# Performance work log

Measured on AMD Instinct MI355X. Metric: run time of the kernel, lower is better.

Reference implementation:

```python
import jax, jax.numpy as jnp
import numpy as np

N = 65536   # number of GP locations
M = 64      # max ancestor set size (contiguous window A(i) = {i-M+1..i})
B = 16384   # minibatch size


def setup_inputs() -> dict:
    rng = np.random.default_rng(0)
    i = np.arange(N)
    # CSR row lengths: U (lower-tri) row i has cols {max(0,i-M+1)..i}; V (upper-tri) row j has cols {j..min(j+M-1,N-1)}
    row_len_u = np.minimum(i + 1, M)
    row_len_v = np.minimum(M, N - i)
    crow_u = np.concatenate([[0], np.cumsum(row_len_u)]).astype(np.int32)
    crow_v = np.concatenate([[0], np.cumsum(row_len_v)]).astype(np.int32)
    nnz = int(crow_u[-1])  # 4192288, same for both matrices
    # off-diagonals small, diagonals near 1 (kept positive for logDet and solve stability)
    U_values = (rng.standard_normal(nnz) * 0.1).astype(np.float32)
    U_values[crow_u[1:] - 1] = rng.uniform(0.8, 1.2, N).astype(np.float32)  # last entry of row i = (i,i)
    V_values = (rng.standard_normal(nnz) * 0.1).astype(np.float32)
    V_values[crow_v[:-1]] = rng.uniform(0.8, 1.2, N).astype(np.float32)    # first entry of row i = (i,i)
    mean = (rng.standard_normal(N) * 0.5).astype(np.float32)
    mean_post = (rng.standard_normal(N) * 0.5).astype(np.float32)
    y = rng.standard_normal(N).astype(np.float32)
    mini_indices = rng.integers(0, N, B).astype(np.int32)
    return {
        'U_values': jnp.asarray(U_values),
        'V_values': jnp.asarray(V_values),
        'mean': jnp.asarray(mean),
        'mean_post': jnp.asarray(mean_post),
        'y': jnp.asarray(y),
        'noise': jnp.float32(0.1),
        'mini_indices': jnp.asarray(mini_indices),
        'crow_u': jnp.asarray(crow_u),
        'crow_v': jnp.asarray(crow_v),
    }


def reference(U_values, V_values, mean, mean_post, y, noise, mini_indices, crow_u, crow_v):
    nnz = U_values.shape[0]
    g = mini_indices                       # [B] selected rows
    L = jnp.minimum(g + 1, M)              # n_anc per selected row
    p = jnp.arange(M)
    valid = p[None, :] >= (M - L)[:, None]                 # [B,M] right-aligned validity mask
    anc = g[:, None] - (M - 1 - p)[None, :]                # global ancestor index at padded slot p
    anc_c = jnp.clip(anc, 0, N - 1)

    # get_sub_rows(UTrans): row g entries at A(g), right-aligned into [B,M]
    u_idx = crow_u[g][:, None] + (p[None, :] - (M - L)[:, None])
    U_sub = jnp.where(valid, U_values[jnp.clip(u_idx, 0, nnz - 1)], 0.0)

    # ragged mean difference gather (masked scatter in the original)
    md = jnp.where(valid, (mean - mean_post)[anc_c], 0.0)  # [B,M]

    # get_sub_mat(V, unit_diag=True): V[A(g),A(g)] bottom-right aligned, identity padding
    jrow = anc_c[:, :, None]                               # global row index of block row r
    icol = anc_c[:, None, :]                               # global col index of block col c
    vidx = crow_v[jrow] + (icol - jrow)                    # CSR value index of V[jrow, icol]
    blk_mask = (valid[:, :, None] & valid[:, None, :]
                & (p[None, :, None] <= p[None, None, :]))  # upper-tri of active block
    eye = jnp.eye(M, dtype=U_values.dtype)
    V_sub = jnp.where(blk_mask, V_values[jnp.clip(vidx, 0, nnz - 1)], eye[None, :, :])  # [B,M,M]

    # batched triangular solves
    ej = jnp.zeros((B, M), U_values.dtype).at[:, -1].set(1.0)
    sol_e = jax.scipy.linalg.solve_triangular(V_sub, ej[:, :, None], lower=False)
    marginalVarPost = jnp.sum(sol_e * sol_e, axis=(1, 2))  # [B]
    sol_u = jax.scipy.linalg.solve_triangular(V_sub, U_sub[:, :, None], lower=False)
    innerCov = -0.5 * jnp.sum(sol_u * sol_u)

    innerMean = -0.5 * jnp.sum(jnp.sum(U_sub * md, axis=1) ** 2)

    # log-determinant terms from diagonal gathers
    logDet = (jnp.sum(jnp.log(U_values[crow_u[g + 1] - 1]))
              - jnp.sum(jnp.log(V_values[crow_v[g]])))

    # Gaussian expected likelihood (noise is not None branch)
    resid = y[g] - mean_post[g]
    ell = (-0.5 * B * jnp.log(2.0 * jnp.pi * noise)
           - (jnp.sum(resid * resid) + jnp.sum(marginalVarPost)) / (2.0 * noise))

    return logDet + innerMean + innerCov + ell
```

## Files before the change

### kernel.cpp

```cpp
#include <hip/hip_runtime.h>
#include <math.h>

constexpr int kN = 65536;
constexpr int kB = 16384;
constexpr int kTileW = 2560;

static __device__ __forceinline__ float bcastf(float v, int lane) {
    union { float f; int i; } u;
    u.f = v;
    u.i = __builtin_amdgcn_readlane(u.i, lane);
    return u.f;
}

static __device__ __forceinline__ void gload_lds16(const float* g, float* l) {
    __builtin_amdgcn_global_load_lds(
        (const __attribute__((address_space(1))) void*)g,
        (__attribute__((address_space(3))) void*)l, 16, 0, 0);
}
static __device__ __forceinline__ void gload_lds4(const float* g, float* l) {
    __builtin_amdgcn_global_load_lds(
        (const __attribute__((address_space(1))) void*)g,
        (__attribute__((address_space(3))) void*)l, 4, 0, 0);
}

static __device__ __forceinline__ int row_start(int j) {
    const int t = j >> 4;
    return 1024 * t - 128 * t * (t - 1) + (64 - 16 * t) * (j - 16 * t);
}

static __device__ __forceinline__ bool is_hot(int g) {
    return (g >= 63) && (g <= kN - 63);
}

__global__ __launch_bounds__(64) void gp_solve_kernel(
    const float* __restrict__ Uv,
    const float* __restrict__ Vv,
    const float* __restrict__ mean,
    const float* __restrict__ mean_post,
    const float* __restrict__ y,
    const int*   __restrict__ gidx,
    const int*   __restrict__ crow_u,
    const int*   __restrict__ crow_v,
    const float* __restrict__ noise,
    float*       __restrict__ partial)
{
    __shared__ __align__(16) float myl[kTileW];

    const int lane = (int)threadIdx.x;
    const int b    = (int)blockIdx.x;
    const int g    = gidx[b];

    const int  anc = g - 63 + lane;
    const bool vl  = (anc >= 0);

    const int L  = (g + 1 < 64) ? (g + 1) : 64;
    const int ub = (g >= 63) ? (2016 + 64 * (g - 63)) : crow_u[g];

    float uval = 0.0f, md = 0.0f;
    if (vl) {
        uval = Uv[ub + lane - (64 - L)];
        md   = mean[anc] - mean_post[anc];
    }
    const float yg  = y[g];
    const float mpg = mean_post[g];

    if (is_hot(g)) {
        const float* base = Vv + 64 * (g - 63);
        {
            const float* src = base + 4 * lane;
            #pragma unroll
            for (int k = 0; k < 4; ++k)
                gload_lds16(src + 256 * k, myl + 256 * k);
        }
        #pragma unroll
        for (int k = 0; k < 3; ++k) {
            const int w   = 256 * k + 4 * lane;
            const int jj  = ((w >> 4) * 171) >> 9;
            const int col = w - 48 * jj;
            gload_lds16(base + 64 * (16 + jj) + col, myl + 1024 + 256 * k);
        }
        #pragma unroll
        for (int k = 0; k < 2; ++k) {
            const int w = 256 * k + 4 * lane;
            gload_lds16(base + 64 * (32 + (w >> 5)) + (w & 31), myl + 1792 + 256 * k);
        }
        {
            const int w = 4 * lane;
            gload_lds16(base + 64 * (48 + (w >> 4)) + (w & 15), myl + 2304);
        }
    } else {
        int rowbase = 0;
        if (vl) rowbase = crow_v[anc];
        for (int j = 0; j < 64; ++j) {
            const int rbj = __builtin_amdgcn_readlane(rowbase, j);
            const int dst = row_start(j);
            if (lane < 64 - j) {
                if (g - 63 + j >= 0)
                    gload_lds4(Vv + rbj + lane, myl + dst);
                else
                    myl[dst + lane] = 0.0f;
            }
        }
    }
    asm volatile("s_waitcnt vmcnt(0) lgkmcnt(0)" ::: "memory");

    const int rs = row_start(lane);
    const float d0   = myl[rs];
    const float diag = vl ? d0 : 1.0f;
    const float invd = 1.0f / diag;

    const float* vrow = myl + (rs - lane);
    float v[64];
    #pragma unroll
    for (int i = 0; i < 64; i += 2) {
        const float a0 = vrow[i];
        const float a1 = vrow[i + 1];
        v[i]     = a0 * invd;
        v[i + 1] = a1 * invd;
    }

    float r_e = (lane == 63) ? invd : 0.0f;
    float r_u = uval * invd;
    float acc_e = 0.0f, acc_u = 0.0f;

    #pragma unroll
    for (int i = 63; i >= 0; --i) {
        const float s_e = bcastf(r_e, i);
        const float s_u = bcastf(r_u, i);
        r_e = fmaf(-v[i], s_e, r_e);
        r_u = fmaf(-v[i], s_u, r_u);
        acc_e = fmaf(s_e, s_e, acc_e);
        acc_u = fmaf(s_u, s_u, acc_u);
    }

    float dot = uval * md;
    #pragma unroll
    for (int m = 1; m < 64; m <<= 1)
        dot += __shfl_xor(dot, m, 64);

    const float ulast  = bcastf(uval, 63);
    const float vfirst = bcastf(diag, 63);

    if (lane == 0) {
        const float resid = yg - mpg;
        const float inv2n = 0.5f / noise[0];
        partial[b] = __logf(ulast) - __logf(vfirst)
                   - 0.5f * dot * dot
                   - 0.5f * acc_u
                   - (resid * resid + acc_e) * inv2n;
    }
}

__global__ __launch_bounds__(1024) void gp_reduce_kernel(
    const float* __restrict__ partial,
    const float* __restrict__ noise,
    float*       __restrict__ out)
{
    __shared__ float ws[16];
    const int t = (int)threadIdx.x;
    float a = 0.0f;
    #pragma unroll
    for (int k = 0; k < 4; ++k) {
        const float4 p = reinterpret_cast<const float4*>(partial)[t + 1024 * k];
        a += (p.x + p.y) + (p.z + p.w);
    }
    #pragma unroll
    for (int m = 1; m < 64; m <<= 1)
        a += __shfl_xor(a, m, 64);
    if ((t & 63) == 0) ws[t >> 6] = a;
    __syncthreads();
    if (t == 0) {
        float tot = 0.0f;
        #pragma unroll
        for (int k = 0; k < 16; ++k) tot += ws[k];
        tot += -0.5f * (float)kB * logf(2.0f * 3.14159265358979323846f * noise[0]);
        out[0] = tot;
    }
}

extern "C" void kernel_launch(void* const* d_in, const int* in_sizes, int n_in,
                              void* d_out, int out_size, void* d_ws, size_t ws_size,
                              hipStream_t stream)
{
    const float* Uv        = (const float*)d_in[0];
    const float* Vv        = (const float*)d_in[1];
    const float* mean      = (const float*)d_in[2];
    const float* mean_post = (const float*)d_in[3];
    const float* y         = (const float*)d_in[4];
    const float* noise     = (const float*)d_in[5];
    const int*   gidx      = (const int*)d_in[6];
    const int*   crow_u    = (const int*)d_in[7];
    const int*   crow_v    = (const int*)d_in[8];
    float* partial = (float*)d_ws;

    gp_solve_kernel<<<dim3(kB), dim3(64), 0, stream>>>(
        Uv, Vv, mean, mean_post, y, gidx, crow_u, crow_v, noise, partial);
    gp_reduce_kernel<<<dim3(1), dim3(1024), 0, stream>>>(
        partial, noise, (float*)d_out);
}
```

Baseline: 36.94 us.

## Bucket minibatch rows by index range to share V tiles across solves

Adds a single-block counting sort that groups minibatch indices into 1024 buckets of 64 rows. Each bucket block loads one contiguous 8192-float V slab into LDS and runs all of its rows' triangular solves from that slab, instead of every row fetching its own 64x64 window. Tail-bucket rows go to a separate per-row cold kernel capped at 512 entries, and the final reduce is shrunk. This removes redundant global traffic for overlapping windows, at the cost of two extra launches, a serial sort block, and load imbalance across buckets. If more than 512 indices land in the last bucket, the overflow is silently dropped.

New measurement: 53.06 us. 1.44x slower.

```diff
diff --git a/kernel.cpp b/kernel.cpp
--- a/kernel.cpp
+++ b/kernel.cpp
@@ -3,6 +3,9 @@
 
 constexpr int kN = 65536;
 constexpr int kB = 16384;
+constexpr int kNB = 1024;
+constexpr int kBufW = 8192;
+constexpr int kColdCap = 512;
 constexpr int kTileW = 2560;
 
 static __device__ __forceinline__ float bcastf(float v, int lane) {
@@ -27,34 +30,198 @@
     const int t = j >> 4;
     return 1024 * t - 128 * t * (t - 1) + (64 - 16 * t) * (j - 16 * t);
 }
-
 static __device__ __forceinline__ bool is_hot(int g) {
     return (g >= 63) && (g <= kN - 63);
 }
 
-__global__ __launch_bounds__(64) void gp_solve_kernel(
+__global__ __launch_bounds__(1024) void gp_sort_kernel(
+    const int* __restrict__ gidx,
+    int* __restrict__ sortedg, int* __restrict__ start,
+    int* __restrict__ coldg, int* __restrict__ coldcnt)
+{
+    __shared__ int hist[kNB];
+    __shared__ int wsum[16];
+    __shared__ int coldc;
+    const int t = (int)threadIdx.x, lane = t & 63, w = t >> 6;
+    hist[t] = 0;
+    if (t == 0) coldc = 0;
+    __syncthreads();
+    int gs[16];
+    #pragma unroll
+    for (int k = 0; k < 16; ++k) {
+        gs[k] = gidx[t + 1024 * k];
+        const int bkt = gs[k] >> 6;
+        if (bkt < kNB - 1) atomicAdd(&hist[bkt], 1);
+    }
+    __syncthreads();
+    const int v = hist[t];
+    int x = v;
+    #pragma unroll
+    for (int d = 1; d < 64; d <<= 1) {
+        const int nn = __shfl_up(x, d, 64);
+        if (lane >= d) x += nn;
+    }
+    if (lane == 63) wsum[w] = x;
+    __syncthreads();
+    if (t == 0) {
+        int acc = 0;
+        #pragma unroll
+        for (int k = 0; k < 16; ++k) { const int sv = wsum[k]; wsum[k] = acc; acc += sv; }
+    }
+    __syncthreads();
+    const int excl = x - v + wsum[w];
+    start[t] = excl;
+    if (t == kNB - 1) start[kNB] = excl + v;
+    __syncthreads();
+    hist[t] = excl;
+    __syncthreads();
+    #pragma unroll
+    for (int k = 0; k < 16; ++k) {
+        const int g = gs[k], bkt = g >> 6;
+        if (bkt < kNB - 1) {
+            const int p = atomicAdd(&hist[bkt], 1);
+            sortedg[p] = g;
+        } else {
+            const int p = atomicAdd(&coldc, 1);
+            if (p < kColdCap) coldg[p] = g;
+        }
+    }
+    __syncthreads();
+    if (t == 0) coldcnt[0] = (coldc < kColdCap) ? coldc : kColdCap;
+}
+
+__global__ __launch_bounds__(256) void gp_bucket_kernel(
     const float* __restrict__ Uv,
     const float* __restrict__ Vv,
     const float* __restrict__ mean,
     const float* __restrict__ mean_post,
     const float* __restrict__ y,
-    const int*   __restrict__ gidx,
+    const int*   __restrict__ crow_u,
+    const float* __restrict__ noise,
+    const int*   __restrict__ sortedg,
+    const int*   __restrict__ start,
+    float*       __restrict__ partial)
+{
+    __shared__ __align__(16) float buf[kBufW];
+    __shared__ float cred[4];
+
+    const int tid  = (int)threadIdx.x, lane = tid & 63, wid = tid >> 6;
+    const int bid  = (int)blockIdx.x;
+    const int b    = ((bid & 7) << 7) | (bid >> 3);
+    const int s    = start[b];
+    const int n    = start[b + 1] - s;
+    if (n == 0) { if (tid == 0) partial[b] = 0.0f; return; }
+
+    const float inv2n = 0.5f / noise[0];
+
+    if (b > 0) {
+        const float* src = Vv + 64 * (64 * b - 63);
+        #pragma unroll
+        for (int k = 0; k < 8; ++k) {
+            const int ow = 1024 * k + 256 * wid;
+            gload_lds16(src + ow + 4 * lane, buf + ow);
+        }
+    } else {
+        #pragma unroll
+        for (int k = 0; k < 8; ++k) {
+            const int wd = 1024 * k + 4 * tid;
+            float4 val = make_float4(0.0f, 0.0f, 0.0f, 0.0f);
+            if (wd >= 4032)
+                val = *reinterpret_cast<const float4*>(Vv + (wd - 4032));
+            *reinterpret_cast<float4*>(buf + wd) = val;
+        }
+    }
+    asm volatile("s_waitcnt vmcnt(0) lgkmcnt(0)" ::: "memory");
+    __syncthreads();
+
+    float accum = 0.0f;
+    for (int e = wid; e < n; e += 4) {
+        const int g   = sortedg[s + e];
+        const int off = g - 64 * b;
+        const int anc = g - 63 + lane;
+        const bool vl = (anc >= 0);
+        const int  L  = (g + 1 < 64) ? (g + 1) : 64;
+        const int  ub = (g >= 63) ? (2016 + 64 * (g - 63)) : crow_u[g];
+
+        float uval = 0.0f, md = 0.0f;
+        if (vl) {
+            uval = Uv[ub + lane - (64 - L)];
+            md   = mean[anc] - mean_post[anc];
+        }
+        const float yv  = y[g];
+        const float mpv = mean_post[g];
+
+        const int l = off + lane;
+        const float d0 = buf[64 * l];
+        const float invd = vl ? (1.0f / d0) : 0.0f;
+
+        const float* vrow = buf + (64 * l - lane);
+        float v[64];
+        #pragma unroll
+        for (int i = 0; i < 64; i += 2) {
+            const float a0 = vrow[i];
+            const float a1 = vrow[i + 1];
+            v[i]     = a0 * invd;
+            v[i + 1] = a1 * invd;
+        }
+
+        float r_e = (lane == 63) ? invd : 0.0f;
+        float r_u = uval * invd;
+        float acc_e = 0.0f, acc_u = 0.0f;
+        #pragma unroll
+        for (int i = 63; i >= 0; --i) {
+            const float s_e = bcastf(r_e, i);
+            const float s_u = bcastf(r_u, i);
+            r_e = fmaf(-v[i], s_e, r_e);
+            r_u = fmaf(-v[i], s_u, r_u);
+            acc_e = fmaf(s_e, s_e, acc_e);
+            acc_u = fmaf(s_u, s_u, acc_u);
+        }
+
+        float dot = uval * md;
+        #pragma unroll
+        for (int m = 1; m < 64; m <<= 1)
+            dot += __shfl_xor(dot, m, 64);
+
+        const float ulast  = bcastf(uval, 63);
+        const float vfirst = bcastf(d0, 63);
+        const float resid  = yv - mpv;
+        accum += __logf(ulast) - __logf(vfirst)
+               - 0.5f * dot * dot
+               - 0.5f * acc_u
+               - (resid * resid + acc_e) * inv2n;
+    }
+
+    if (lane == 0) cred[wid] = accum;
+    __syncthreads();
+    if (tid == 0)
+        partial[b] = (cred[0] + cred[1]) + (cred[2] + cred[3]);
+}
+
+__global__ __launch_bounds__(64) void gp_cold_kernel(
+    const float* __restrict__ Uv,
+    const float* __restrict__ Vv,
+    const float* __restrict__ mean,
+    const float* __restrict__ mean_post,
+    const float* __restrict__ y,
     const int*   __restrict__ crow_u,
     const int*   __restrict__ crow_v,
     const float* __restrict__ noise,
-    float*       __restrict__ partial)
+    const int*   __restrict__ coldg,
+    const int*   __restrict__ coldcnt,
+    float*       __restrict__ partialC)
 {
     __shared__ __align__(16) float myl[kTileW];
-
     const int lane = (int)threadIdx.x;
-    const int b    = (int)blockIdx.x;
-    const int g    = gidx[b];
+    const int i    = (int)blockIdx.x;
+    const int cnt  = coldcnt[0];
+    if (i >= cnt) { if (lane == 0) partialC[i] = 0.0f; return; }
+    const int g = coldg[i];
 
     const int  anc = g - 63 + lane;
     const bool vl  = (anc >= 0);
-
-    const int L  = (g + 1 < 64) ? (g + 1) : 64;
-    const int ub = (g >= 63) ? (2016 + 64 * (g - 63)) : crow_u[g];
+    const int  L   = (g + 1 < 64) ? (g + 1) : 64;
+    const int  ub  = (g >= 63) ? (2016 + 64 * (g - 63)) : crow_u[g];
 
     float uval = 0.0f, md = 0.0f;
     if (vl) {
@@ -66,12 +233,9 @@
 
     if (is_hot(g)) {
         const float* base = Vv + 64 * (g - 63);
-        {
-            const float* src = base + 4 * lane;
-            #pragma unroll
-            for (int k = 0; k < 4; ++k)
-                gload_lds16(src + 256 * k, myl + 256 * k);
-        }
+        { const float* src = base + 4 * lane;
+          #pragma unroll
+          for (int k = 0; k < 4; ++k) gload_lds16(src + 256 * k, myl + 256 * k); }
         #pragma unroll
         for (int k = 0; k < 3; ++k) {
             const int w   = 256 * k + 4 * lane;
@@ -84,10 +248,8 @@
             const int w = 256 * k + 4 * lane;
             gload_lds16(base + 64 * (32 + (w >> 5)) + (w & 31), myl + 1792 + 256 * k);
         }
-        {
-            const int w = 4 * lane;
-            gload_lds16(base + 64 * (48 + (w >> 4)) + (w & 15), myl + 2304);
-        }
+        { const int w = 4 * lane;
+          gload_lds16(base + 64 * (48 + (w >> 4)) + (w & 15), myl + 2304); }
     } else {
         int rowbase = 0;
         if (vl) rowbase = crow_v[anc];
@@ -95,10 +257,8 @@
             const int rbj = __builtin_amdgcn_readlane(rowbase, j);
             const int dst = row_start(j);
             if (lane < 64 - j) {
-                if (g - 63 + j >= 0)
-                    gload_lds4(Vv + rbj + lane, myl + dst);
-                else
-                    myl[dst + lane] = 0.0f;
+                if (g - 63 + j >= 0) gload_lds4(Vv + rbj + lane, myl + dst);
+                else                 myl[dst + lane] = 0.0f;
             }
         }
     }
@@ -107,28 +267,27 @@
     const int rs = row_start(lane);
     const float d0   = myl[rs];
     const float diag = vl ? d0 : 1.0f;
-    const float invd = 1.0f / diag;
+    const float invd = vl ? (1.0f / d0) : 0.0f;
 
     const float* vrow = myl + (rs - lane);
     float v[64];
     #pragma unroll
-    for (int i = 0; i < 64; i += 2) {
-        const float a0 = vrow[i];
-        const float a1 = vrow[i + 1];
-        v[i]     = a0 * invd;
-        v[i + 1] = a1 * invd;
+    for (int i2 = 0; i2 < 64; i2 += 2) {
+        const float a0 = vrow[i2];
+        const float a1 = vrow[i2 + 1];
+        v[i2]     = a0 * invd;
+        v[i2 + 1] = a1 * invd;
     }
 
     float r_e = (lane == 63) ? invd : 0.0f;
     float r_u = uval * invd;
     float acc_e = 0.0f, acc_u = 0.0f;
-
-    #pragma unroll
-    for (int i = 63; i >= 0; --i) {
-        const float s_e = bcastf(r_e, i);
-        const float s_u = bcastf(r_u, i);
-        r_e = fmaf(-v[i], s_e, r_e);
-        r_u = fmaf(-v[i], s_u, r_u);
+    #pragma unroll
+    for (int i2 = 63; i2 >= 0; --i2) {
+        const float s_e = bcastf(r_e, i2);
+        const float s_u = bcastf(r_u, i2);
+        r_e = fmaf(-v[i2], s_e, r_e);
+        r_u = fmaf(-v[i2], s_u, r_u);
         acc_e = fmaf(s_e, s_e, acc_e);
         acc_u = fmaf(s_u, s_u, acc_u);
     }
@@ -140,29 +299,27 @@
 
     const float ulast  = bcastf(uval, 63);
     const float vfirst = bcastf(diag, 63);
-
     if (lane == 0) {
         const float resid = yg - mpg;
         const float inv2n = 0.5f / noise[0];
-        partial[b] = __logf(ulast) - __logf(vfirst)
-                   - 0.5f * dot * dot
-                   - 0.5f * acc_u
-                   - (resid * resid + acc_e) * inv2n;
-    }
-}
-
-__global__ __launch_bounds__(1024) void gp_reduce_kernel(
-    const float* __restrict__ partial,
+        partialC[i] = __logf(ulast) - __logf(vfirst)
+                    - 0.5f * dot * dot
+                    - 0.5f * acc_u
+                    - (resid * resid + acc_e) * inv2n;
+    }
+}
+
+__global__ __launch_bounds__(512) void gp_reduce_kernel(
+    const float* __restrict__ partials,
     const float* __restrict__ noise,
     float*       __restrict__ out)
 {
-    __shared__ float ws[16];
+    __shared__ float ws[8];
     const int t = (int)threadIdx.x;
     float a = 0.0f;
-    #pragma unroll
-    for (int k = 0; k < 4; ++k) {
-        const float4 p = reinterpret_cast<const float4*>(partial)[t + 1024 * k];
-        a += (p.x + p.y) + (p.z + p.w);
+    if (t < 384) {
+        const float4 p = reinterpret_cast<const float4*>(partials)[t];
+        a = (p.x + p.y) + (p.z + p.w);
     }
     #pragma unroll
     for (int m = 1; m < 64; m <<= 1)
@@ -172,7 +329,7 @@
     if (t == 0) {
         float tot = 0.0f;
         #pragma unroll
-        for (int k = 0; k < 16; ++k) tot += ws[k];
+        for (int k = 0; k < 8; ++k) tot += ws[k];
         tot += -0.5f * (float)kB * logf(2.0f * 3.14159265358979323846f * noise[0]);
         out[0] = tot;
     }
@@ -191,10 +348,21 @@
     const int*   gidx      = (const int*)d_in[6];
     const int*   crow_u    = (const int*)d_in[7];
     const int*   crow_v    = (const int*)d_in[8];
-    float* partial = (float*)d_ws;
-
-    gp_solve_kernel<<<dim3(kB), dim3(64), 0, stream>>>(
-        Uv, Vv, mean, mean_post, y, gidx, crow_u, crow_v, noise, partial);
-    gp_reduce_kernel<<<dim3(1), dim3(1024), 0, stream>>>(
+
+    int* ws_i      = (int*)d_ws;
+    int* sortedg   = ws_i;
+    int* start     = ws_i + 16384;
+    int* coldg     = ws_i + 16384 + 1025;
+    int* coldcnt   = ws_i + 16384 + 1025 + 512;
+    float* partial  = (float*)(ws_i + 17924);
+    float* partialC = partial + kNB;
+
+    gp_sort_kernel<<<dim3(1), dim3(1024), 0, stream>>>(
+        gidx, sortedg, start, coldg, coldcnt);
+    gp_bucket_kernel<<<dim3(kNB), dim3(256), 0, stream>>>(
+        Uv, Vv, mean, mean_post, y, crow_u, noise, sortedg, start, partial);
+    gp_cold_kernel<<<dim3(kColdCap), dim3(64), 0, stream>>>(
+        Uv, Vv, mean, mean_post, y, crow_u, crow_v, noise, coldg, coldcnt, partialC);
+    gp_reduce_kernel<<<dim3(1), dim3(512), 0, stream>>>(
         partial, noise, (float*)d_out);
 }
```

## Bucket minibatch rows by 64-row tile and share V tile in LDS

Applied to the files above, without the earlier changes.

Adds a counting sort (histogram, scan, scatter) that groups the minibatch indices into 1024 buckets of 64 consecutive rows. One block per bucket loads the 127-row V window into LDS once, and its four wavefronts then solve every selected row in that bucket from the shared tile. This cuts redundant global reads of overlapping V windows, but adds four small extra launches plus a memset, atomics, and possible load imbalance across buckets. The final reduction shrinks to 1024 partials.

Result: slower. 49.13 us (+33.0%).

```diff
diff --git a/kernel.cpp b/kernel.cpp
--- a/kernel.cpp
+++ b/kernel.cpp
@@ -3,7 +3,8 @@
 
 constexpr int kN = 65536;
 constexpr int kB = 16384;
-constexpr int kTileW = 2560;
+constexpr int kNB = 1024;
+constexpr int kBufW = 8192;
 
 static __device__ __forceinline__ float bcastf(float v, int lane) {
     union { float f; int i; } u;
@@ -17,162 +18,183 @@
         (const __attribute__((address_space(1))) void*)g,
         (__attribute__((address_space(3))) void*)l, 16, 0, 0);
 }
-static __device__ __forceinline__ void gload_lds4(const float* g, float* l) {
-    __builtin_amdgcn_global_load_lds(
-        (const __attribute__((address_space(1))) void*)g,
-        (__attribute__((address_space(3))) void*)l, 4, 0, 0);
-}
-
-static __device__ __forceinline__ int row_start(int j) {
-    const int t = j >> 4;
-    return 1024 * t - 128 * t * (t - 1) + (64 - 16 * t) * (j - 16 * t);
-}
-
-static __device__ __forceinline__ bool is_hot(int g) {
-    return (g >= 63) && (g <= kN - 63);
-}
-
-__global__ __launch_bounds__(64) void gp_solve_kernel(
+
+__global__ __launch_bounds__(1024) void gp_hist_kernel(
+    const int* __restrict__ gidx, int* __restrict__ hist)
+{
+    const int i = (int)blockIdx.x * 1024 + (int)threadIdx.x;
+    atomicAdd(&hist[gidx[i] >> 6], 1);
+}
+
+__global__ __launch_bounds__(1024) void gp_scan_kernel(
+    int* __restrict__ hist, int* __restrict__ start)
+{
+    __shared__ int wsum[16];
+    const int t = (int)threadIdx.x, lane = t & 63, w = t >> 6;
+    const int v = hist[t];
+    int x = v;
+    #pragma unroll
+    for (int d = 1; d < 64; d <<= 1) {
+        const int nn = __shfl_up(x, d, 64);
+        if (lane >= d) x += nn;
+    }
+    if (lane == 63) wsum[w] = x;
+    __syncthreads();
+    if (t == 0) {
+        int acc = 0;
+        #pragma unroll
+        for (int k = 0; k < 16; ++k) { const int sv = wsum[k]; wsum[k] = acc; acc += sv; }
+    }
+    __syncthreads();
+    const int excl = x - v + wsum[w];
+    start[t] = excl;
+    if (t == kNB - 1) start[kNB] = excl + v;
+    hist[t] = excl;
+}
+
+__global__ __launch_bounds__(1024) void gp_scatter_kernel(
+    const int* __restrict__ gidx, int* __restrict__ cursor,
+    int* __restrict__ sortedg)
+{
+    const int i = (int)blockIdx.x * 1024 + (int)threadIdx.x;
+    const int g = gidx[i];
+    const int p = atomicAdd(&cursor[g >> 6], 1);
+    sortedg[p] = g;
+}
+
+__global__ __launch_bounds__(256) void gp_bucket_kernel(
     const float* __restrict__ Uv,
     const float* __restrict__ Vv,
     const float* __restrict__ mean,
     const float* __restrict__ mean_post,
     const float* __restrict__ y,
-    const int*   __restrict__ gidx,
     const int*   __restrict__ crow_u,
     const int*   __restrict__ crow_v,
     const float* __restrict__ noise,
+    const int*   __restrict__ sortedg,
+    const int*   __restrict__ start,
     float*       __restrict__ partial)
 {
-    __shared__ __align__(16) float myl[kTileW];
-
-    const int lane = (int)threadIdx.x;
-    const int b    = (int)blockIdx.x;
-    const int g    = gidx[b];
-
-    const int  anc = g - 63 + lane;
-    const bool vl  = (anc >= 0);
-
-    const int L  = (g + 1 < 64) ? (g + 1) : 64;
-    const int ub = (g >= 63) ? (2016 + 64 * (g - 63)) : crow_u[g];
-
-    float uval = 0.0f, md = 0.0f;
-    if (vl) {
-        uval = Uv[ub + lane - (64 - L)];
-        md   = mean[anc] - mean_post[anc];
-    }
-    const float yg  = y[g];
-    const float mpg = mean_post[g];
-
-    if (is_hot(g)) {
-        const float* base = Vv + 64 * (g - 63);
-        {
-            const float* src = base + 4 * lane;
-            #pragma unroll
-            for (int k = 0; k < 4; ++k)
-                gload_lds16(src + 256 * k, myl + 256 * k);
-        }
-        #pragma unroll
-        for (int k = 0; k < 3; ++k) {
-            const int w   = 256 * k + 4 * lane;
-            const int jj  = ((w >> 4) * 171) >> 9;
-            const int col = w - 48 * jj;
-            gload_lds16(base + 64 * (16 + jj) + col, myl + 1024 + 256 * k);
-        }
-        #pragma unroll
-        for (int k = 0; k < 2; ++k) {
-            const int w = 256 * k + 4 * lane;
-            gload_lds16(base + 64 * (32 + (w >> 5)) + (w & 31), myl + 1792 + 256 * k);
-        }
-        {
-            const int w = 4 * lane;
-            gload_lds16(base + 64 * (48 + (w >> 4)) + (w & 15), myl + 2304);
+    __shared__ __align__(16) float buf[kBufW];
+    __shared__ float cred[4];
+
+    const int tid  = (int)threadIdx.x, lane = tid & 63, wid = tid >> 6;
+    const int bid  = (int)blockIdx.x;
+    const int b    = ((bid & 7) << 7) | (bid >> 3);
+    const int s    = start[b];
+    const int n    = start[b + 1] - s;
+    if (n == 0) { if (tid == 0) partial[b] = 0.0f; return; }
+
+    const float inv2n = 0.5f / noise[0];
+
+    if (b >= 1 && b <= kNB - 2) {
+        const float* src = Vv + 64 * (64 * b - 63);
+        #pragma unroll
+        for (int k = 0; k < 8; ++k) {
+            const int ow = 1024 * k + 256 * wid;
+            gload_lds16(src + ow + 4 * lane, buf + ow);
+        }
+    } else if (b == 0) {
+        #pragma unroll
+        for (int k = 0; k < 8; ++k) {
+            const int wd = 1024 * k + 4 * tid;
+            float4 val = make_float4(0.0f, 0.0f, 0.0f, 0.0f);
+            if (wd >= 4032)
+                val = *reinterpret_cast<const float4*>(Vv + (wd - 4032));
+            *reinterpret_cast<float4*>(buf + wd) = val;
         }
     } else {
-        int rowbase = 0;
-        if (vl) rowbase = crow_v[anc];
-        for (int j = 0; j < 64; ++j) {
-            const int rbj = __builtin_amdgcn_readlane(rowbase, j);
-            const int dst = row_start(j);
-            if (lane < 64 - j) {
-                if (g - 63 + j >= 0)
-                    gload_lds4(Vv + rbj + lane, myl + dst);
-                else
-                    myl[dst + lane] = 0.0f;
-            }
+        for (int j = wid; j < 127; j += 4) {
+            const int r  = 64 * (kNB - 1) - 63 + j;
+            const int rb = crow_v[r];
+            const int w  = (kN - r < 64) ? (kN - r) : 64;
+            const float val = (lane < w) ? Vv[rb + lane] : 0.0f;
+            buf[64 * j + lane] = val;
         }
     }
     asm volatile("s_waitcnt vmcnt(0) lgkmcnt(0)" ::: "memory");
-
-    const int rs = row_start(lane);
-    const float d0   = myl[rs];
-    const float diag = vl ? d0 : 1.0f;
-    const float invd = 1.0f / diag;
-
-    const float* vrow = myl + (rs - lane);
-    float v[64];
-    #pragma unroll
-    for (int i = 0; i < 64; i += 2) {
-        const float a0 = vrow[i];
-        const float a1 = vrow[i + 1];
-        v[i]     = a0 * invd;
-        v[i + 1] = a1 * invd;
-    }
-
-    float r_e = (lane == 63) ? invd : 0.0f;
-    float r_u = uval * invd;
-    float acc_e = 0.0f, acc_u = 0.0f;
-
-    #pragma unroll
-    for (int i = 63; i >= 0; --i) {
-        const float s_e = bcastf(r_e, i);
-        const float s_u = bcastf(r_u, i);
-        r_e = fmaf(-v[i], s_e, r_e);
-        r_u = fmaf(-v[i], s_u, r_u);
-        acc_e = fmaf(s_e, s_e, acc_e);
-        acc_u = fmaf(s_u, s_u, acc_u);
-    }
-
-    float dot = uval * md;
-    #pragma unroll
-    for (int m = 1; m < 64; m <<= 1)
-        dot += __shfl_xor(dot, m, 64);
-
-    const float ulast  = bcastf(uval, 63);
-    const float vfirst = bcastf(diag, 63);
-
-    if (lane == 0) {
-        const float resid = yg - mpg;
-        const float inv2n = 0.5f / noise[0];
-        partial[b] = __logf(ulast) - __logf(vfirst)
-                   - 0.5f * dot * dot
-                   - 0.5f * acc_u
-                   - (resid * resid + acc_e) * inv2n;
-    }
-}
-
-__global__ __launch_bounds__(1024) void gp_reduce_kernel(
+    __syncthreads();
+
+    float accum = 0.0f;
+    for (int e = wid; e < n; e += 4) {
+        const int g   = sortedg[s + e];
+        const int off = g - 64 * b;
+        const int anc = g - 63 + lane;
+        const bool vl = (anc >= 0);
+        const int  L  = (g + 1 < 64) ? (g + 1) : 64;
+        const int  ub = (g >= 63) ? (2016 + 64 * (g - 63)) : crow_u[g];
+
+        float uval = 0.0f, md = 0.0f;
+        if (vl) {
+            uval = Uv[ub + lane - (64 - L)];
+            md   = mean[anc] - mean_post[anc];
+        }
+        const float yv  = y[g];
+        const float mpv = mean_post[g];
+
+        const int l = off + lane;
+        const float d0 = buf[64 * l];
+        const float invd = vl ? (1.0f / d0) : 0.0f;
+
+        const float* vrow = buf + (64 * l - lane);
+        float v[64];
+        #pragma unroll
+        for (int i = 0; i < 64; i += 2) {
+            const float a0 = vrow[i];
+            const float a1 = vrow[i + 1];
+            v[i]     = a0 * invd;
+            v[i + 1] = a1 * invd;
+        }
+
+        float r_e = (lane == 63) ? invd : 0.0f;
+        float r_u = uval * invd;
+        float acc_e = 0.0f, acc_u = 0.0f;
+        #pragma unroll
+        for (int i = 63; i >= 0; --i) {
+            const float s_e = bcastf(r_e, i);
+            const float s_u = bcastf(r_u, i);
+            r_e = fmaf(-v[i], s_e, r_e);
+            r_u = fmaf(-v[i], s_u, r_u);
+            acc_e = fmaf(s_e, s_e, acc_e);
+            acc_u = fmaf(s_u, s_u, acc_u);
+        }
+
+        float dot = uval * md;
+        #pragma unroll
+        for (int m = 1; m < 64; m <<= 1)
+            dot += __shfl_xor(dot, m, 64);
+
+        const float ulast  = bcastf(uval, 63);
+        const float vfirst = bcastf(d0, 63);
+        const float resid  = yv - mpv;
+        accum += __logf(ulast) - __logf(vfirst)
+               - 0.5f * dot * dot
+               - 0.5f * acc_u
+               - (resid * resid + acc_e) * inv2n;
+    }
+
+    if (lane == 0) cred[wid] = accum;
+    __syncthreads();
+    if (tid == 0)
+        partial[b] = (cred[0] + cred[1]) + (cred[2] + cred[3]);
+}
+
+__global__ __launch_bounds__(256) void gp_reduce_kernel(
     const float* __restrict__ partial,
     const float* __restrict__ noise,
     float*       __restrict__ out)
 {
-    __shared__ float ws[16];
+    __shared__ float ws[4];
     const int t = (int)threadIdx.x;
-    float a = 0.0f;
-    #pragma unroll
-    for (int k = 0; k < 4; ++k) {
-        const float4 p = reinterpret_cast<const float4*>(partial)[t + 1024 * k];
-        a += (p.x + p.y) + (p.z + p.w);
-    }
+    const float4 p = reinterpret_cast<const float4*>(partial)[t];
+    float a = (p.x + p.y) + (p.z + p.w);
     #pragma unroll
     for (int m = 1; m < 64; m <<= 1)
         a += __shfl_xor(a, m, 64);
     if ((t & 63) == 0) ws[t >> 6] = a;
     __syncthreads();
     if (t == 0) {
-        float tot = 0.0f;
-        #pragma unroll
-        for (int k = 0; k < 16; ++k) tot += ws[k];
+        float tot = (ws[0] + ws[1]) + (ws[2] + ws[3]);
         tot += -0.5f * (float)kB * logf(2.0f * 3.14159265358979323846f * noise[0]);
         out[0] = tot;
     }
@@ -191,10 +213,19 @@
     const int*   gidx      = (const int*)d_in[6];
     const int*   crow_u    = (const int*)d_in[7];
     const int*   crow_v    = (const int*)d_in[8];
-    float* partial = (float*)d_ws;
-
-    gp_solve_kernel<<<dim3(kB), dim3(64), 0, stream>>>(
-        Uv, Vv, mean, mean_post, y, gidx, crow_u, crow_v, noise, partial);
-    gp_reduce_kernel<<<dim3(1), dim3(1024), 0, stream>>>(
+
+    int* ws_i     = (int*)d_ws;
+    int* sortedg  = ws_i;
+    int* hist     = ws_i + 16384;
+    int* start    = ws_i + 16384 + 1024;
+    float* partial = (float*)(ws_i + 18448);
+
+    hipMemsetAsync(hist, 0, kNB * sizeof(int), stream);
+    gp_hist_kernel   <<<dim3(kB / 1024), dim3(1024), 0, stream>>>(gidx, hist);
+    gp_scan_kernel   <<<dim3(1),         dim3(1024), 0, stream>>>(hist, start);
+    gp_scatter_kernel<<<dim3(kB / 1024), dim3(1024), 0, stream>>>(gidx, hist, sortedg);
+    gp_bucket_kernel <<<dim3(kNB),       dim3(256),  0, stream>>>(
+        Uv, Vv, mean, mean_post, y, crow_u, crow_v, noise, sortedg, start, partial);
+    gp_reduce_kernel <<<dim3(1),         dim3(256),  0, stream>>>(
         partial, noise, (float*)d_out);
 }
```
